# Kernel tuning notes

Measured on AMD Instinct MI355X. Metric: run time of the kernel, lower is better.

Reference implementation:

```python
import jax, jax.numpy as jnp
import numpy as np

N_NODES = 20000
N_EDGES = 320000
HEADS = 16
NEG_SLOPE = 0.2


def _gat_conv(x, src, dst, W, a_src, a_dst, b, heads, out_ch):
    # x: [N, F_in]; src/dst: [E'] (self-loops already appended)
    N = x.shape[0]
    h = (x @ W).reshape(N, heads, out_ch)                  # [N, H, C]
    alpha_s = jnp.sum(h * a_src, axis=-1)                  # [N, H]
    alpha_d = jnp.sum(h * a_dst, axis=-1)                  # [N, H]
    e = jax.nn.leaky_relu(alpha_s[src] + alpha_d[dst], NEG_SLOPE)  # [E', H]
    # segment softmax over edges grouped by destination node
    m = jax.ops.segment_max(e, dst, num_segments=N)        # [N, H]
    ex = jnp.exp(e - m[dst])
    denom = jax.ops.segment_sum(ex, dst, num_segments=N)
    alpha = ex / (denom[dst] + 1e-16)                      # [E', H]
    msg = h[src] * alpha[:, :, None]                       # [E', H, C]
    out = jax.ops.segment_sum(msg, dst, num_segments=N)    # [N, H, C]
    return out.reshape(N, heads * out_ch) + b


def _forward(x, edge_index, params):
    N = x.shape[0]
    loops = jnp.arange(N, dtype=edge_index.dtype)
    src = jnp.concatenate([edge_index[0], loops])
    dst = jnp.concatenate([edge_index[1], loops])
    for i, (W, a_s, a_d, b, out_ch) in enumerate(params):
        x = _gat_conv(x, src, dst, W, a_s, a_d, b, HEADS, out_ch)
        if i < len(params) - 1:
            x = jax.nn.relu(x)
    return jnp.sum(x, axis=0, keepdims=True)               # [1, 768]


def setup_inputs() -> dict:
    key = jax.random.key(0)
    ks = jax.random.split(key, 32)
    hid, heads, out_c = 64, HEADS, 3
    dims = [(3, hid), (hid * heads, hid), (hid * heads, hid), (hid * heads, hid), (hid * heads, hid), (hid * heads, out_c * heads)]
    inp = {}
    inp["x"] = jax.random.normal(ks[0], (N_NODES, 3), dtype=jnp.float32)
    inp["edge_index"] = jax.random.randint(ks[1], (2, N_EDGES), 0, N_NODES, dtype=jnp.int64)
    k = 2
    for li, (fin, c) in enumerate(dims, start=1):
        inp[f"W{li}"] = jax.random.normal(ks[k], (fin, heads * c), dtype=jnp.float32) * 0.1; k += 1
        inp[f"a{li}s"] = jax.random.normal(ks[k], (heads, c), dtype=jnp.float32) * 0.1; k += 1
        inp[f"a{li}d"] = jax.random.normal(ks[k], (heads, c), dtype=jnp.float32) * 0.1; k += 1
        inp[f"b{li}"] = jnp.zeros((heads * c,), dtype=jnp.float32)
    return inp


def reference(x, edge_index, W1, a1s, a1d, b1, W2, a2s, a2d, b2, W3, a3s, a3d, b3, W4, a4s, a4d, b4, W5, a5s, a5d, b5, W6, a6s, a6d, b6):
    params = [
        (W1, a1s, a1d, b1, 64), (W2, a2s, a2d, b2, 64), (W3, a3s, a3d, b3, 64),
        (W4, a4s, a4d, b4, 64), (W5, a5s, a5d, b5, 64), (W6, a6s, a6d, b6, 48),
    ]
    return _forward(x, edge_index, params)
```

## Files before the change

### kernel.cpp

```cpp
#include <hip/hip_runtime.h>
#include <cstddef>
#include <cstdint>

#define N_NODES 20000
#define N_EDGES 320000
#define E_TOT   (N_EDGES + N_NODES)
#define HEADS   16

typedef __bf16 bf16;
typedef __attribute__((ext_vector_type(8))) __bf16 bf16x8;
typedef __attribute__((ext_vector_type(4))) __bf16 bf16x4;
typedef __attribute__((ext_vector_type(4))) float  f32x4;

__device__ __forceinline__ void gll16(const void* g, void* l) {
    __builtin_amdgcn_global_load_lds(
        (const __attribute__((address_space(1))) unsigned int*)g,
        (__attribute__((address_space(3))) unsigned int*)l, 16, 0, 0);
}

__global__ __launch_bounds__(256)
void k_lin1(const float* __restrict__ x, const float* __restrict__ W,
            const float* __restrict__ aS, const float* __restrict__ aD,
            bf16* __restrict__ hg, float* __restrict__ as_,
            float* __restrict__ ad_) {
    int n = blockIdx.x;
    int t = threadIdx.x;
    int f0 = t * 4, hd = t >> 4;
    float x0 = x[n*3+0], x1 = x[n*3+1], x2 = x[n*3+2];
    float v[4];
    bf16x4 hv;
#pragma unroll
    for (int c = 0; c < 4; ++c) {
        int f = f0 + c;
        v[c] = x0*W[f] + x1*W[1024+f] + x2*W[2048+f];
        hv[c] = (bf16)v[c];
    }
    *reinterpret_cast<bf16x4*>(&hg[(size_t)n * 1024 + f0]) = hv;
    float ps = 0.f, pd = 0.f;
    int cb = (t & 15) * 4;
#pragma unroll
    for (int c = 0; c < 4; ++c) {
        ps = fmaf(v[c], aS[hd*64 + cb + c], ps);
        pd = fmaf(v[c], aD[hd*64 + cb + c], pd);
    }
#pragma unroll
    for (int off = 1; off < 16; off <<= 1) {
        ps += __shfl_xor(ps, off);
        pd += __shfl_xor(pd, off);
    }
    if ((t & 15) == 0) {
        as_[n*16 + hd] = ps;
        ad_[n*16 + hd] = pd;
    }
}

__global__ __launch_bounds__(256)
void k_convW(const float* __restrict__ W, bf16* __restrict__ Th,
             bf16* __restrict__ Tl, int M) {
    __shared__ float t[32][33];
    int m0 = blockIdx.x * 32, k0 = blockIdx.y * 32;
    int j = threadIdx.x & 31, i0 = threadIdx.x >> 5;
#pragma unroll
    for (int s = 0; s < 4; ++s) {
        int i = i0 + s * 8;
        t[i][j] = W[(size_t)(k0 + i) * M + m0 + j];
    }
    __syncthreads();
#pragma unroll
    for (int s = 0; s < 4; ++s) {
        int i = i0 + s * 8;
        float v = t[j][i];
        bf16 hi = (bf16)v;
        bf16 lo = (bf16)(v - (float)hi);
        Th[(size_t)(m0 + i) * 1024 + k0 + j] = hi;
        Tl[(size_t)(m0 + i) * 1024 + k0 + j] = lo;
    }
}

template<bool FUSE>
__global__ __launch_bounds__(256, 2)
void k_gemm3(const bf16* __restrict__ Ah,
             const bf16* __restrict__ Bh, const bf16* __restrict__ Bl,
             float* __restrict__ Cf, bf16* __restrict__ Ch,
             const float* __restrict__ aS, const float* __restrict__ aD,
             float* __restrict__ as_, float* __restrict__ ad_,
             int N, int M) {
    __shared__ __align__(16) bf16 sAh[128 * 32];
    __shared__ __align__(16) bf16 sBh[128 * 32];
    __shared__ __align__(16) bf16 sBl[128 * 32];

    const int tid  = threadIdx.x;
    const int wid  = tid >> 6, lane = tid & 63;
    const int wr   = wid >> 1, wc = wid & 1;
    const int col0 = blockIdx.x * 128, row0 = blockIdx.y * 128;

    f32x4 acc[4][4] = {};

    const int rl = lane >> 2;
    const int gg = lane & 3;
    const int rb0 = wid * 32;
    const int lrow = lane & 15, g4 = lane >> 4;

    for (int k0 = 0; k0 < 1024; k0 += 32) {
#pragma unroll
        for (int half = 0; half < 2; ++half) {
            int rt = rb0 + half * 16 + rl;
            int kc = (gg ^ ((rt >> 1) & 3)) * 8;
            size_t lbase = (size_t)(rb0 + half * 16) * 32;
            int ar = row0 + rt; if (ar >= N) ar = N - 1;
            gll16(Ah + (size_t)ar * 1024 + k0 + kc, sAh + lbase);
            int br = col0 + rt;
            gll16(Bh + (size_t)br * 1024 + k0 + kc, sBh + lbase);
            gll16(Bl + (size_t)br * 1024 + k0 + kc, sBl + lbase);
        }
        __syncthreads();

        bf16x8 ah[4], bh[4], bl[4];
#pragma unroll
        for (int m = 0; m < 4; ++m) {
            int r = wr * 64 + m * 16 + lrow;
            int off = r * 32 + ((g4 ^ ((r >> 1) & 3)) * 8);
            ah[m] = *(const bf16x8*)&sAh[off];
        }
#pragma unroll
        for (int n = 0; n < 4; ++n) {
            int r = wc * 64 + n * 16 + lrow;
            int off = r * 32 + ((g4 ^ ((r >> 1) & 3)) * 8);
            bh[n] = *(const bf16x8*)&sBh[off];
            bl[n] = *(const bf16x8*)&sBl[off];
        }
#pragma unroll
        for (int m = 0; m < 4; ++m)
#pragma unroll
            for (int n = 0; n < 4; ++n) {
                acc[m][n] = __builtin_amdgcn_mfma_f32_16x16x32_bf16(ah[m], bh[n], acc[m][n], 0, 0, 0);
                acc[m][n] = __builtin_amdgcn_mfma_f32_16x16x32_bf16(ah[m], bl[n], acc[m][n], 0, 0, 0);
            }
        __syncthreads();
    }

#pragma unroll
    for (int m = 0; m < 4; ++m) {
#pragma unroll
        for (int n = 0; n < 4; ++n) {
            int col = col0 + wc * 64 + n * 16 + lrow;
#pragma unroll
            for (int q = 0; q < 4; ++q) {
                int row = row0 + wr * 64 + m * 16 + g4 * 4 + q;
                if (row < N) {
                    float v = acc[m][n][q];
                    if (!FUSE) Cf[(size_t)row * M + col] = v;
                    Ch[(size_t)row * M + col] = (bf16)v;
                }
            }
        }
    }

    if (FUSE) {
        const int hd = blockIdx.x * 2 + wc;
        float asv[4], adv[4];
#pragma unroll
        for (int n = 0; n < 4; ++n) {
            asv[n] = aS[hd * 64 + n * 16 + lrow];
            adv[n] = aD[hd * 64 + n * 16 + lrow];
        }
        float ps[4][4], pd[4][4];
#pragma unroll
        for (int m = 0; m < 4; ++m)
#pragma unroll
            for (int q = 0; q < 4; ++q) {
                float s = 0.f, d = 0.f;
#pragma unroll
                for (int n = 0; n < 4; ++n) {
                    s = fmaf(acc[m][n][q], asv[n], s);
                    d = fmaf(acc[m][n][q], adv[n], d);
                }
                ps[m][q] = s; pd[m][q] = d;
            }
#pragma unroll
        for (int off = 1; off < 16; off <<= 1) {
#pragma unroll
            for (int m = 0; m < 4; ++m)
#pragma unroll
                for (int q = 0; q < 4; ++q) {
                    ps[m][q] += __shfl_xor(ps[m][q], off);
                    pd[m][q] += __shfl_xor(pd[m][q], off);
                }
        }
        if (lrow == 0) {
#pragma unroll
            for (int m = 0; m < 4; ++m)
#pragma unroll
                for (int q = 0; q < 4; ++q) {
                    int row = row0 + wr * 64 + m * 16 + g4 * 4 + q;
                    if (row < N) {
                        as_[row * 16 + hd] = ps[m][q];
                        ad_[row * 16 + hd] = pd[m][q];
                    }
                }
        }
    }
}

__global__ __launch_bounds__(256)
void k_alpha(const float* __restrict__ h, const float* __restrict__ a_s,
             const float* __restrict__ a_d, float* __restrict__ as_out,
             float* __restrict__ ad_out, int C, int M) {
    int pair = blockIdx.x * 4 + (threadIdx.x >> 6);
    int lane = threadIdx.x & 63;
    if (pair >= N_NODES * HEADS) return;
    int n = pair >> 4, hd = pair & 15;
    float vs = 0.f, vd = 0.f;
    if (lane < C) {
        float hv = h[(size_t)n * M + hd * C + lane];
        vs = hv * a_s[hd * C + lane];
        vd = hv * a_d[hd * C + lane];
    }
#pragma unroll
    for (int off = 32; off > 0; off >>= 1) {
        vs += __shfl_down(vs, off);
        vd += __shfl_down(vd, off);
    }
    if (lane == 0) { as_out[pair] = vs; ad_out[pair] = vd; }
}

__global__ void k_zero_i(int* __restrict__ p, int n) {
    int t = blockIdx.x * 256 + threadIdx.x;
    if (t < n) p[t] = 0;
}
__global__ void k_hist(const int* __restrict__ ei, int* __restrict__ deg) {
    int e = blockIdx.x * 256 + threadIdx.x;
    if (e >= E_TOT) return;
    int d = (e < N_EDGES) ? ei[N_EDGES + e] : e - N_EDGES;
    atomicAdd(&deg[d], 1);
}
__global__ __launch_bounds__(256)
void k_scan(const int* __restrict__ deg, int* __restrict__ rowstart,
            int* __restrict__ cursor) {
    __shared__ int sh[256];
    int carry = 0;
    for (int base = 0; base < N_NODES; base += 256) {
        int i = base + threadIdx.x;
        int v = (i < N_NODES) ? deg[i] : 0;
        sh[threadIdx.x] = v;
        __syncthreads();
        for (int off = 1; off < 256; off <<= 1) {
            int t = (threadIdx.x >= off) ? sh[threadIdx.x - off] : 0;
            __syncthreads();
            sh[threadIdx.x] += t;
            __syncthreads();
        }
        if (i < N_NODES) {
            int excl = carry + sh[threadIdx.x] - v;
            rowstart[i] = excl;
            cursor[i] = excl;
        }
        carry += sh[255];
        __syncthreads();
    }
    if (threadIdx.x == 0) rowstart[N_NODES] = carry;
}
__global__ void k_scatter(const int* __restrict__ ei, int* __restrict__ cursor,
                          int* __restrict__ csr_src) {
    int e = blockIdx.x * 256 + threadIdx.x;
    if (e >= E_TOT) return;
    int s, d;
    if (e < N_EDGES) { s = ei[e]; d = ei[N_EDGES + e]; }
    else             { s = d = e - N_EDGES; }
    int slot = atomicAdd(&cursor[d], 1);
    csr_src[slot] = s;
}

__global__ __launch_bounds__(256)
void k_agg1024(const bf16* __restrict__ hg, const int* __restrict__ rowstart,
               const int* __restrict__ csr_src, const float* __restrict__ as_,
               const float* __restrict__ ad_, const float* __restrict__ bias,
               bf16* __restrict__ oh) {
    int n = blockIdx.x * 2 + (threadIdx.x >> 7);
    int tloc = threadIdx.x & 127;
    int f0 = tloc * 8;
    int hd = tloc >> 3;
    int s0 = rowstart[n], s1 = rowstart[n + 1];
    float adv = ad_[n * 16 + hd];
    float m = -1e30f, den = 0.f;
    float acc[8] = {};
    for (int j = s0; j < s1; ++j) {
        int s = csr_src[j];
        float v = as_[s * 16 + hd] + adv;
        v = v > 0.f ? v : 0.2f * v;
        bf16x8 hv = *reinterpret_cast<const bf16x8*>(&hg[(size_t)s * 1024 + f0]);
        float nm = fmaxf(m, v);
        float rm = __expf(m - nm);
        float re = __expf(v - nm);
        den = den * rm + re;
#pragma unroll
        for (int c = 0; c < 8; ++c)
            acc[c] = fmaf(acc[c], rm, re * (float)hv[c]);
        m = nm;
    }
    float inv = 1.f / (den + 1e-16f);
    bf16x8 vh;
#pragma unroll
    for (int c = 0; c < 8; ++c) {
        float r = fmaxf(fmaf(acc[c], inv, bias[f0 + c]), 0.f);
        vh[c] = (bf16)r;
    }
    *reinterpret_cast<bf16x8*>(&oh[(size_t)n * 1024 + f0]) = vh;
}

__global__ __launch_bounds__(256)
void k_agg768(const bf16* __restrict__ hg, const int* __restrict__ rowstart,
              const int* __restrict__ csr_src, const float* __restrict__ as_,
              const float* __restrict__ ad_, const float* __restrict__ bias,
              float* __restrict__ out) {
    int n = blockIdx.x * 2 + (threadIdx.x >> 7);
    int tloc = threadIdx.x & 127;
    if (tloc >= 96) return;
    int f0 = tloc * 8;
    int hd = f0 / 48;
    int s0 = rowstart[n], s1 = rowstart[n + 1];
    float adv = ad_[n * 16 + hd];
    float m = -1e30f, den = 0.f;
    float acc[8] = {};
    for (int j = s0; j < s1; ++j) {
        int s = csr_src[j];
        float v = as_[s * 16 + hd] + adv;
        v = v > 0.f ? v : 0.2f * v;
        bf16x8 hv = *reinterpret_cast<const bf16x8*>(&hg[(size_t)s * 768 + f0]);
        float nm = fmaxf(m, v);
        float rm = __expf(m - nm);
        float re = __expf(v - nm);
        den = den * rm + re;
#pragma unroll
        for (int c = 0; c < 8; ++c)
            acc[c] = fmaf(acc[c], rm, re * (float)hv[c]);
        m = nm;
    }
    float inv = 1.f / (den + 1e-16f);
#pragma unroll
    for (int c = 0; c < 8; ++c)
        out[(size_t)n * 768 + f0 + c] = fmaf(acc[c], inv, bias[f0 + c]);
}

__global__ __launch_bounds__(256)
void k_colsum(const float* __restrict__ x, float* __restrict__ out) {
    int f = blockIdx.x * 256 + threadIdx.x;
    int chunk = blockIdx.y;
    int n0 = chunk * 625, n1 = n0 + 625;
    float s = 0.f;
    for (int n = n0; n < n1; ++n) s += x[(size_t)n * 768 + f];
    atomicAdd(&out[f], s);
}

extern "C" void kernel_launch(void* const* d_in, const int* in_sizes, int n_in,
                              void* d_out, int out_size, void* d_ws, size_t ws_size,
                              hipStream_t stream) {
    const float* x0 = (const float*)d_in[0];
    const int*   ei = (const int*)d_in[1];

    char* w = (char*)d_ws;
    float* xB  = (float*)w;
    float* xOut = (float*)w;
    w += (size_t)N_NODES * 1024 * sizeof(float);
    bf16*  hgat = (bf16*)w; w += (size_t)N_NODES * 1024 * sizeof(bf16);
    bf16*  x_hi = (bf16*)w; w += (size_t)N_NODES * 1024 * sizeof(bf16);
    float* as_  = (float*)w; w += (size_t)N_NODES * HEADS * sizeof(float);
    float* ad_  = (float*)w; w += (size_t)N_NODES * HEADS * sizeof(float);
    bf16* Wt_hi = (bf16*)w; w += (size_t)1024 * 1024 * sizeof(bf16);
    bf16* Wt_lo = (bf16*)w; w += (size_t)1024 * 1024 * sizeof(bf16);
    int* deg      = (int*)w; w += N_NODES * sizeof(int);
    int* rowstart = (int*)w; w += (N_NODES + 1) * sizeof(int);
    int* cursor   = (int*)w; w += N_NODES * sizeof(int);
    int* csr_src  = (int*)w; w += E_TOT * sizeof(int);

    k_zero_i<<<(N_NODES + 255) / 256, 256, 0, stream>>>(deg, N_NODES);
    k_hist<<<(E_TOT + 255) / 256, 256, 0, stream>>>(ei, deg);
    k_scan<<<1, 256, 0, stream>>>(deg, rowstart, cursor);
    k_scatter<<<(E_TOT + 255) / 256, 256, 0, stream>>>(ei, cursor, csr_src);

    for (int l = 0; l < 6; ++l) {
        const float* W  = (const float*)d_in[2 + 4 * l + 0];
        const float* aS = (const float*)d_in[2 + 4 * l + 1];
        const float* aD = (const float*)d_in[2 + 4 * l + 2];
        const float* bv = (const float*)d_in[2 + 4 * l + 3];
        int M = (l == 5) ? 768 : 1024;

        if (l == 0) {
            k_lin1<<<N_NODES, 256, 0, stream>>>(x0, W, aS, aD, hgat, as_, ad_);
        } else {
            dim3 tg(M / 32, 32);
            k_convW<<<tg, 256, 0, stream>>>(W, Wt_hi, Wt_lo, M);
            dim3 grid(M / 128, (N_NODES + 127) / 128);
            if (l < 5) {
                k_gemm3<true><<<grid, 256, 0, stream>>>(
                    x_hi, Wt_hi, Wt_lo, nullptr, hgat, aS, aD, as_, ad_,
                    N_NODES, M);
            } else {
                k_gemm3<false><<<grid, 256, 0, stream>>>(
                    x_hi, Wt_hi, Wt_lo, xB, hgat, nullptr, nullptr,
                    nullptr, nullptr, N_NODES, M);
                k_alpha<<<(N_NODES * HEADS + 3) / 4, 256, 0, stream>>>(
                    xB, aS, aD, as_, ad_, 48, 768);
            }
        }
        if (l < 5) {
            k_agg1024<<<N_NODES / 2, 256, 0, stream>>>(
                hgat, rowstart, csr_src, as_, ad_, bv, x_hi);
        } else {
            k_agg768<<<N_NODES / 2, 256, 0, stream>>>(
                hgat, rowstart, csr_src, as_, ad_, bv, xOut);
        }
    }

    hipMemsetAsync(d_out, 0, (size_t)out_size * sizeof(float), stream);
    dim3 cgrid(3, 32);
    k_colsum<<<cgrid, 256, 0, stream>>>(xOut, (float*)d_out);
}
```

Measured before the change: 1.316 ms.

## Drop low-bf16 weight correction in hidden layers and retile aggregation by feature slice

For layers 2-5 the GEMM now uses only the high bf16 part of the weights, skipping the second MFMA and the extra B-tile load that compensated for bf16 rounding. The last layer keeps the two-part split. Separately, the 1024-wide aggregation is remapped so each block handles a 128-feature slice for 16 nodes instead of all features for 2 nodes, which changes gather locality and block count. The precision drop halves the hidden-layer MFMA work but adds rounding error to the weights.

```diff
diff --git a/kernel.cpp b/kernel.cpp
--- a/kernel.cpp
+++ b/kernel.cpp
@@ -71,13 +71,12 @@
         int i = i0 + s * 8;
         float v = t[j][i];
         bf16 hi = (bf16)v;
-        bf16 lo = (bf16)(v - (float)hi);
         Th[(size_t)(m0 + i) * 1024 + k0 + j] = hi;
-        Tl[(size_t)(m0 + i) * 1024 + k0 + j] = lo;
-    }
-}
-
-template<bool FUSE>
+        if (Tl) Tl[(size_t)(m0 + i) * 1024 + k0 + j] = (bf16)(v - (float)hi);
+    }
+}
+
+template<bool FUSE, bool TWOB>
 __global__ __launch_bounds__(256, 2)
 void k_gemm3(const bf16* __restrict__ Ah,
              const bf16* __restrict__ Bh, const bf16* __restrict__ Bl,
@@ -87,7 +86,7 @@
              int N, int M) {
     __shared__ __align__(16) bf16 sAh[128 * 32];
     __shared__ __align__(16) bf16 sBh[128 * 32];
-    __shared__ __align__(16) bf16 sBl[128 * 32];
+    __shared__ __align__(16) bf16 sBl[TWOB ? 128 * 32 : 8];
 
     const int tid  = threadIdx.x;
     const int wid  = tid >> 6, lane = tid & 63;
@@ -111,7 +110,7 @@
             gll16(Ah + (size_t)ar * 1024 + k0 + kc, sAh + lbase);
             int br = col0 + rt;
             gll16(Bh + (size_t)br * 1024 + k0 + kc, sBh + lbase);
-            gll16(Bl + (size_t)br * 1024 + k0 + kc, sBl + lbase);
+            if (TWOB) gll16(Bl + (size_t)br * 1024 + k0 + kc, sBl + lbase);
         }
         __syncthreads();
 
@@ -127,14 +126,15 @@
             int r = wc * 64 + n * 16 + lrow;
             int off = r * 32 + ((g4 ^ ((r >> 1) & 3)) * 8);
             bh[n] = *(const bf16x8*)&sBh[off];
-            bl[n] = *(const bf16x8*)&sBl[off];
+            if (TWOB) bl[n] = *(const bf16x8*)&sBl[off];
         }
 #pragma unroll
         for (int m = 0; m < 4; ++m)
 #pragma unroll
             for (int n = 0; n < 4; ++n) {
                 acc[m][n] = __builtin_amdgcn_mfma_f32_16x16x32_bf16(ah[m], bh[n], acc[m][n], 0, 0, 0);
-                acc[m][n] = __builtin_amdgcn_mfma_f32_16x16x32_bf16(ah[m], bl[n], acc[m][n], 0, 0, 0);
+                if (TWOB)
+                    acc[m][n] = __builtin_amdgcn_mfma_f32_16x16x32_bf16(ah[m], bl[n], acc[m][n], 0, 0, 0);
             }
         __syncthreads();
     }
@@ -276,10 +276,11 @@
                const int* __restrict__ csr_src, const float* __restrict__ as_,
                const float* __restrict__ ad_, const float* __restrict__ bias,
                bf16* __restrict__ oh) {
-    int n = blockIdx.x * 2 + (threadIdx.x >> 7);
-    int tloc = threadIdx.x & 127;
-    int f0 = tloc * 8;
-    int hd = tloc >> 3;
+    int slice = blockIdx.x;
+    int n = blockIdx.y * 16 + (threadIdx.x >> 4);
+    int sub = threadIdx.x & 15;
+    int f0 = slice * 128 + sub * 8;
+    int hd = f0 >> 6;
     int s0 = rowstart[n], s1 = rowstart[n + 1];
     float adv = ad_[n * 16 + hd];
     float m = -1e30f, den = 0.f;
@@ -389,14 +390,15 @@
             k_lin1<<<N_NODES, 256, 0, stream>>>(x0, W, aS, aD, hgat, as_, ad_);
         } else {
             dim3 tg(M / 32, 32);
-            k_convW<<<tg, 256, 0, stream>>>(W, Wt_hi, Wt_lo, M);
             dim3 grid(M / 128, (N_NODES + 127) / 128);
             if (l < 5) {
-                k_gemm3<true><<<grid, 256, 0, stream>>>(
-                    x_hi, Wt_hi, Wt_lo, nullptr, hgat, aS, aD, as_, ad_,
+                k_convW<<<tg, 256, 0, stream>>>(W, Wt_hi, nullptr, M);
+                k_gemm3<true, false><<<grid, 256, 0, stream>>>(
+                    x_hi, Wt_hi, nullptr, nullptr, hgat, aS, aD, as_, ad_,
                     N_NODES, M);
             } else {
-                k_gemm3<false><<<grid, 256, 0, stream>>>(
+                k_convW<<<tg, 256, 0, stream>>>(W, Wt_hi, Wt_lo, M);
+                k_gemm3<false, true><<<grid, 256, 0, stream>>>(
                     x_hi, Wt_hi, Wt_lo, xB, hgat, nullptr, nullptr,
                     nullptr, nullptr, N_NODES, M);
                 k_alpha<<<(N_NODES * HEADS + 3) / 4, 256, 0, stream>>>(
@@ -404,7 +406,8 @@
             }
         }
         if (l < 5) {
-            k_agg1024<<<N_NODES / 2, 256, 0, stream>>>(
+            dim3 agrid(8, N_NODES / 16);
+            k_agg1024<<<agrid, 256, 0, stream>>>(
                 hgat, rowstart, csr_src, as_, ad_, bv, x_hi);
         } else {
             k_agg768<<<N_NODES / 2, 256, 0, stream>>>(
```

Measured after the change: 1.218 ms. 1.08x faster.
